# Kernel tuning notes

Measured on AMD Instinct MI355X. Metric: run time of the kernel, lower is better.

Reference implementation:

```python
import jax, jax.numpy as jnp
import numpy as np

N_HEAD = 4
D_K = 64
D_V = 64
D_MODEL = 256
LN_EPS = 1e-5


def setup_inputs() -> dict:
    key = jax.random.key(0)
    k1, k2, k3 = jax.random.split(key, 3)
    B, C, H, W = 2, D_MODEL, 64, 64
    q = jax.random.normal(k1, (B, C, H, W), dtype=jnp.float32)
    # w_qkvs: Linear(d_model, n_head*d_k, bias=False), weight [out, in]
    std_qkv = np.sqrt(2.0 / (D_MODEL + D_K))
    w_qkv = jax.random.normal(k2, (N_HEAD * D_K, D_MODEL), dtype=jnp.float32) * std_qkv
    # fc: Linear(n_head*d_v, d_model), xavier-normal-ish init
    std_fc = np.sqrt(2.0 / (N_HEAD * D_V + D_MODEL))
    fc_w = jax.random.normal(k3, (D_MODEL, N_HEAD * D_V), dtype=jnp.float32) * std_fc
    fc_b = jnp.zeros((D_MODEL,), dtype=jnp.float32)
    ln_g = jnp.ones((D_MODEL,), dtype=jnp.float32)
    ln_b = jnp.zeros((D_MODEL,), dtype=jnp.float32)
    return {"q": q, "w_qkv": w_qkv, "fc_w": fc_w, "fc_b": fc_b, "ln_g": ln_g, "ln_b": ln_b}


def reference(q, w_qkv, fc_w, fc_b, ln_g, ln_b):
    B, C, H, W = q.shape
    L = H * W
    # [B, C, H, W] -> [B, L, C]
    x = q.reshape(B, C, L).transpose(0, 2, 1)
    residual = x
    # shared QKV projection (self-attention branch: q == k == v)
    qkv = x @ w_qkv.T                                  # [B, L, nh*dk]
    qh = qkv.reshape(B, L, N_HEAD, D_K).transpose(2, 0, 1, 3)  # [h, B, L, dk]
    scale = jnp.asarray(np.sqrt(D_K), dtype=q.dtype)
    attn = jnp.einsum('hbqd,hbkd->hbqk', qh, qh) / scale       # [h, B, L, L]
    attn = jax.nn.softmax(attn, axis=-1)
    out = jnp.einsum('hbqk,hbkd->hbqd', attn, qh)              # [h, B, L, dv]
    # [h, B, L, dv] -> [B, L, h*dv]
    out = out.transpose(1, 2, 0, 3).reshape(B, L, N_HEAD * D_V)
    out = out @ fc_w.T + fc_b
    out = out + residual
    mu = jnp.mean(out, axis=-1, keepdims=True)
    var = jnp.mean(jnp.square(out - mu), axis=-1, keepdims=True)
    out = (out - mu) / jnp.sqrt(var + LN_EPS) * ln_g + ln_b
    # raw row-major view back to [B, C, H, W] (matches torch .view)
    return out.reshape(B, -1, H, W)
```

## Files before the change

### kernel.cpp

```cpp
#include <hip/hip_runtime.h>

#define L_SEQ 4096
#define DMODEL 256
#define DH 64
#define NKB 16

typedef __attribute__((ext_vector_type(8))) __bf16 bf16x8;
typedef __attribute__((ext_vector_type(4))) float f32x4;
typedef __attribute__((ext_vector_type(8))) unsigned short ushort8v;
typedef __attribute__((ext_vector_type(4))) unsigned short ushort4v;

__device__ __forceinline__ unsigned short f2bf(float f) {
  unsigned u = __builtin_bit_cast(unsigned, f);
  u += 0x7fffu + ((u >> 16) & 1u);
  return (unsigned short)(u >> 16);
}
__device__ __forceinline__ float bf2f(unsigned short h) {
  unsigned u = ((unsigned)h) << 16;
  return __builtin_bit_cast(float, u);
}
__device__ __forceinline__ bf16x8 ld_frag(const unsigned short* p) {
  return __builtin_bit_cast(bf16x8, *(const ushort8v*)p);
}

__global__ __launch_bounds__(256) void k_transpose(const float* __restrict__ q,
                                                   unsigned short* __restrict__ xbf,
                                                   const float* __restrict__ w,
                                                   const float* __restrict__ fcw,
                                                   unsigned short* __restrict__ wbf,
                                                   unsigned short* __restrict__ fcwbf) {
  int bx = blockIdx.x;
  int t = threadIdx.x;
  if (bx >= 512) {
    int i = ((bx - 512) * 256 + t) * 4;
    float4 a = *(const float4*)(w + i);
    float4 b = *(const float4*)(fcw + i);
    ushort4v av = {f2bf(a.x), f2bf(a.y), f2bf(a.z), f2bf(a.w)};
    ushort4v bv = {f2bf(b.x), f2bf(b.y), f2bf(b.z), f2bf(b.w)};
    *(ushort4v*)(wbf + i) = av;
    *(ushort4v*)(fcwbf + i) = bv;
    return;
  }
  __shared__ float T[64 * 65];
  int b = bx >> 8, rest = bx & 255;
  int ct = rest >> 6, lt = rest & 63;
#pragma unroll
  for (int it = 0; it < 4; ++it) {
    int i = (t >> 4) + it * 16;
    int j0 = (t & 15) * 4;
    float4 v = *(const float4*)(q + ((size_t)(b * 256 + ct * 64 + i)) * 4096 + lt * 64 + j0);
    T[i * 65 + j0 + 0] = v.x;
    T[i * 65 + j0 + 1] = v.y;
    T[i * 65 + j0 + 2] = v.z;
    T[i * 65 + j0 + 3] = v.w;
  }
  __syncthreads();
#pragma unroll
  for (int it = 0; it < 2; ++it) {
    int l = (t >> 3) + it * 32;
    int c0 = (t & 7) * 8;
    ushort8v o;
#pragma unroll
    for (int k = 0; k < 8; ++k) o[k] = f2bf(T[(c0 + k) * 65 + l]);
    *(ushort8v*)(xbf + ((size_t)(b * 4096 + lt * 64 + l)) * 256 + ct * 64 + c0) = o;
  }
}

#define KP2 136
__global__ __launch_bounds__(256) void k_qkv(const unsigned short* __restrict__ xbf,
                                             const unsigned short* __restrict__ wbf,
                                             unsigned short* __restrict__ Qh,
                                             unsigned short* __restrict__ QhT) {
  __shared__ unsigned short As[64 * KP2];
  __shared__ unsigned short Bs[64 * KP2];
  int bx = blockIdx.x;
  int mtile = bx >> 2, h = bx & 3;
  int m0 = mtile * 64;
  int b = m0 >> 12, l0 = m0 & 4095;
  int t = threadIdx.x;
  int wv = t >> 6, lane = t & 63, g = lane >> 4, ln = lane & 15;
  f32x4 acc[4] = {};
  for (int kb = 0; kb < 2; ++kb) {
#pragma unroll
    for (int it = 0; it < 4; ++it) {
      int idx = t + it * 256;
      int row = idx >> 4;
      int c0 = (idx & 15) * 8;
      *(ushort8v*)(As + row * KP2 + c0) =
          *(const ushort8v*)(xbf + (size_t)(m0 + row) * 256 + kb * 128 + c0);
      *(ushort8v*)(Bs + row * KP2 + c0) =
          *(const ushort8v*)(wbf + (size_t)(h * 64 + row) * 256 + kb * 128 + c0);
    }
    __syncthreads();
#pragma unroll
    for (int kc = 0; kc < 4; ++kc) {
      bf16x8 a = ld_frag(As + (wv * 16 + ln) * KP2 + kc * 32 + g * 8);
#pragma unroll
      for (int tn = 0; tn < 4; ++tn) {
        bf16x8 bb = ld_frag(Bs + (tn * 16 + ln) * KP2 + kc * 32 + g * 8);
        acc[tn] = __builtin_amdgcn_mfma_f32_16x16x32_bf16(a, bb, acc[tn], 0, 0, 0);
      }
    }
    __syncthreads();
  }
  size_t pbase = (size_t)(b * 4 + h);
#pragma unroll
  for (int tn = 0; tn < 4; ++tn) {
#pragma unroll
    for (int r = 0; r < 4; ++r) {
      int lrow = wv * 16 + g * 4 + r;
      int d = tn * 16 + ln;
      unsigned short bv = f2bf(acc[tn][r]);
      As[lrow * 64 + (((d >> 3) ^ (lrow & 7)) * 8) + (d & 7)] = bv;
      Bs[d * 64 + (((lrow >> 3) ^ (d & 7)) * 8) + (lrow & 7)] = bv;
    }
  }
#pragma unroll
  for (int s = 0; s < 2; ++s) {
    int flat = s * 64 + lane;
    int lrow = wv * 16 + (flat >> 3);
    int c8 = lane & 7;
    ushort8v v = *(const ushort8v*)(As + lrow * 64 + ((c8 ^ (lrow & 7)) * 8));
    *(ushort8v*)(Qh + (pbase * L_SEQ + l0 + lrow) * DH + c8 * 8) = v;
  }
  __syncthreads();
#pragma unroll
  for (int s = 0; s < 2; ++s) {
    int flat = s * 256 + t;
    int drow = flat >> 3;
    int c8 = t & 7;
    ushort8v v = *(const ushort8v*)(Bs + drow * 64 + ((c8 ^ (drow & 7)) * 8));
    *(ushort8v*)(QhT + (pbase * DH + drow) * L_SEQ + l0 + c8 * 8) = v;
  }
}

__global__ __launch_bounds__(256, 2) void k_attn(const unsigned short* __restrict__ Qh,
                                                 const unsigned short* __restrict__ QhT,
                                                 unsigned short* __restrict__ Opart,
                                                 float* __restrict__ Lpart) {
  __shared__ unsigned short Kt[64 * 64];
  __shared__ unsigned short Vt[64 * 64];
  __shared__ unsigned short Pb[256 * 64];
  int bx = blockIdx.x;
  int p = bx & 7;
  int u = bx >> 3;
  int qsup = u & 15, ks = u >> 4;
  int t = threadIdx.x;
  int wv = t >> 6, lane = t & 63, g = lane >> 4, ln = lane & 15;
  const unsigned short* Qp = Qh + (size_t)p * L_SEQ * DH;
  const unsigned short* QTp = QhT + (size_t)p * DH * L_SEQ;
  int q0 = qsup * 256;
  int qw = q0 + wv * 64;

  bf16x8 aQ[4][2];
#pragma unroll
  for (int nt = 0; nt < 4; ++nt)
#pragma unroll
    for (int kc = 0; kc < 2; ++kc)
      aQ[nt][kc] = ld_frag(Qp + (size_t)(qw + nt * 16 + ln) * DH + kc * 32 + g * 8);

  f32x4 oacc[4][4] = {};
  float lacc[4] = {0.f, 0.f, 0.f, 0.f};

  int srow0 = t >> 3, scol0 = t & 7;
  int srow1 = (t + 256) >> 3, scol1 = (t + 256) & 7;
  int sdst0 = srow0 * 64 + ((scol0 ^ (srow0 & 7)) * 8);
  int sdst1 = srow1 * 64 + ((scol1 ^ (srow1 & 7)) * 8);

  ushort8v kreg0, kreg1, vreg0, vreg1;
  {
    int kbase = (ks * NKB) * 64;
    kreg0 = *(const ushort8v*)(Qp + (size_t)(kbase + srow0) * DH + scol0 * 8);
    kreg1 = *(const ushort8v*)(Qp + (size_t)(kbase + srow1) * DH + scol1 * 8);
    vreg0 = *(const ushort8v*)(QTp + (size_t)srow0 * L_SEQ + kbase + scol0 * 8);
    vreg1 = *(const ushort8v*)(QTp + (size_t)srow1 * L_SEQ + kbase + scol1 * 8);
  }

  for (int kb = 0; kb < NKB; ++kb) {
    __syncthreads();
    *(ushort8v*)(Kt + sdst0) = kreg0;
    *(ushort8v*)(Kt + sdst1) = kreg1;
    *(ushort8v*)(Vt + sdst0) = vreg0;
    *(ushort8v*)(Vt + sdst1) = vreg1;
    __syncthreads();
    if (kb + 1 < NKB) {
      int kbase = (ks * NKB + kb + 1) * 64;
      kreg0 = *(const ushort8v*)(Qp + (size_t)(kbase + srow0) * DH + scol0 * 8);
      kreg1 = *(const ushort8v*)(Qp + (size_t)(kbase + srow1) * DH + scol1 * 8);
      vreg0 = *(const ushort8v*)(QTp + (size_t)srow0 * L_SEQ + kbase + scol0 * 8);
      vreg1 = *(const ushort8v*)(QTp + (size_t)srow1 * L_SEQ + kbase + scol1 * 8);
    }
#pragma unroll
    for (int mt = 0; mt < 4; ++mt) {
      int krow = mt * 16 + ln;
      bf16x8 aK0 = ld_frag(Kt + krow * 64 + (((0 * 4 + g) ^ (ln & 7)) * 8));
      bf16x8 aK1 = ld_frag(Kt + krow * 64 + (((1 * 4 + g) ^ (ln & 7)) * 8));
      f32x4 s[4] = {};
#pragma unroll
      for (int nt = 0; nt < 4; ++nt) {
        s[nt] = __builtin_amdgcn_mfma_f32_16x16x32_bf16(aK0, aQ[nt][0], s[nt], 0, 0, 0);
        s[nt] = __builtin_amdgcn_mfma_f32_16x16x32_bf16(aK1, aQ[nt][1], s[nt], 0, 0, 0);
      }
#pragma unroll
      for (int nt = 0; nt < 4; ++nt) {
        float p0 = __expf(fmaf(s[nt][0], 0.125f, -16.0f));
        float p1 = __expf(fmaf(s[nt][1], 0.125f, -16.0f));
        float p2 = __expf(fmaf(s[nt][2], 0.125f, -16.0f));
        float p3 = __expf(fmaf(s[nt][3], 0.125f, -16.0f));
        lacc[nt] += (p0 + p1) + (p2 + p3);
        ushort4v pk = {f2bf(p0), f2bf(p1), f2bf(p2), f2bf(p3)};
        int row = wv * 64 + nt * 16 + ln;
        int addr = row * 64 + (((2 * mt + (g >> 1)) ^ (ln & 7)) * 8) + (g & 1) * 4;
        *(ushort4v*)(Pb + addr) = pk;
      }
    }
#pragma unroll
    for (int kc = 0; kc < 2; ++kc) {
      bf16x8 bV[4];
#pragma unroll
      for (int tn = 0; tn < 4; ++tn)
        bV[tn] = ld_frag(Vt + (tn * 16 + ln) * 64 + (((kc * 4 + g) ^ (ln & 7)) * 8));
#pragma unroll
      for (int mq = 0; mq < 4; ++mq) {
        bf16x8 aP = ld_frag(Pb + (wv * 64 + mq * 16 + ln) * 64 + (((kc * 4 + g) ^ (ln & 7)) * 8));
#pragma unroll
        for (int tn = 0; tn < 4; ++tn)
          oacc[mq][tn] = __builtin_amdgcn_mfma_f32_16x16x32_bf16(aP, bV[tn], oacc[mq][tn], 0, 0, 0);
      }
    }
  }
#pragma unroll
  for (int nt = 0; nt < 4; ++nt) {
    lacc[nt] += __shfl_xor(lacc[nt], 16, 64);
    lacc[nt] += __shfl_xor(lacc[nt], 32, 64);
  }
  size_t pq = (size_t)(ks * 8 + p) * L_SEQ;
  if (g == 0) {
#pragma unroll
    for (int nt = 0; nt < 4; ++nt)
      __builtin_nontemporal_store(lacc[nt], &Lpart[pq + qw + nt * 16 + ln]);
  }
#pragma unroll
  for (int mq = 0; mq < 4; ++mq) {
#pragma unroll
    for (int r = 0; r < 4; ++r) {
      int row = wv * 64 + mq * 16 + g * 4 + r;
#pragma unroll
      for (int tn = 0; tn < 4; ++tn) {
        int d = tn * 16 + ln;
        Pb[row * 64 + (((d >> 3) ^ (row & 7)) * 8) + (d & 7)] = f2bf(oacc[mq][tn][r]);
      }
    }
  }
#pragma unroll
  for (int s = 0; s < 8; ++s) {
    int flat = s * 64 + lane;
    int row = wv * 64 + (flat >> 3);
    int c8 = lane & 7;
    ushort8v v = *(const ushort8v*)(Pb + row * 64 + ((c8 ^ (row & 7)) * 8));
    __builtin_nontemporal_store(v, (ushort8v*)(Opart + (pq + q0 + row) * DH + c8 * 8));
  }
}

#define CP 72
__global__ __launch_bounds__(256) void k_fc(const unsigned short* __restrict__ Opart,
                                            const float* __restrict__ Lpart,
                                            const unsigned short* __restrict__ fcwbf,
                                            const float* __restrict__ qres,
                                            const float* __restrict__ fcb,
                                            const float* __restrict__ lng,
                                            const float* __restrict__ lnb,
                                            float* __restrict__ out) {
  __shared__ unsigned short As[32 * CP];
  __shared__ unsigned short Bs[256 * CP];
  __shared__ float redS[4][32], redQ[4][32], muA[32], rsA[32];
  int bx = blockIdx.x;
  int m0 = bx * 32;
  int b = m0 >> 12, lpart = m0 & 4095;
  int t = threadIdx.x;
  int wv = t >> 6, lane = t & 63, g = lane >> 4, ln = lane & 15;
  f32x4 acc[2][4] = {};
  for (int kb = 0; kb < 4; ++kb) {
    {
      int row = t >> 3, c0 = (t & 7) * 8;
      int q = lpart + row;
      int p = b * 4 + kb;
      float lsum = __builtin_nontemporal_load(&Lpart[(size_t)(0 * 8 + p) * L_SEQ + q]) +
                   __builtin_nontemporal_load(&Lpart[(size_t)(1 * 8 + p) * L_SEQ + q]) +
                   __builtin_nontemporal_load(&Lpart[(size_t)(2 * 8 + p) * L_SEQ + q]) +
                   __builtin_nontemporal_load(&Lpart[(size_t)(3 * 8 + p) * L_SEQ + q]);
      float inv = 1.0f / lsum;
      float a8[8] = {0.f, 0.f, 0.f, 0.f, 0.f, 0.f, 0.f, 0.f};
#pragma unroll
      for (int ksp = 0; ksp < 4; ++ksp) {
        ushort8v v = __builtin_nontemporal_load(
            (const ushort8v*)(Opart + ((size_t)(ksp * 8 + p) * L_SEQ + q) * DH + c0));
#pragma unroll
        for (int j = 0; j < 8; ++j) a8[j] += bf2f(v[j]);
      }
      ushort8v o;
#pragma unroll
      for (int j = 0; j < 8; ++j) o[j] = f2bf(a8[j] * inv);
      *(ushort8v*)(As + row * CP + c0) = o;
    }
#pragma unroll
    for (int it = 0; it < 8; ++it) {
      int idx = t + it * 256;
      int row = idx >> 3, c0 = (idx & 7) * 8;
      *(ushort8v*)(Bs + row * CP + c0) =
          *(const ushort8v*)(fcwbf + (size_t)row * 256 + kb * 64 + c0);
    }
    __syncthreads();
#pragma unroll
    for (int kc = 0; kc < 2; ++kc) {
      bf16x8 a[2], bb[4];
#pragma unroll
      for (int mt = 0; mt < 2; ++mt) a[mt] = ld_frag(As + (mt * 16 + ln) * CP + kc * 32 + g * 8);
#pragma unroll
      for (int tn = 0; tn < 4; ++tn) bb[tn] = ld_frag(Bs + (wv * 64 + tn * 16 + ln) * CP + kc * 32 + g * 8);
#pragma unroll
      for (int mt = 0; mt < 2; ++mt)
#pragma unroll
        for (int tn = 0; tn < 4; ++tn)
          acc[mt][tn] = __builtin_amdgcn_mfma_f32_16x16x32_bf16(a[mt], bb[tn], acc[mt][tn], 0, 0, 0);
    }
    __syncthreads();
  }
  float fb[4], lg[4], lb[4];
#pragma unroll
  for (int tn = 0; tn < 4; ++tn) {
    int o = wv * 64 + tn * 16 + ln;
    fb[tn] = fcb[o]; lg[tn] = lng[o]; lb[tn] = lnb[o];
  }
#pragma unroll
  for (int mt = 0; mt < 2; ++mt) {
    float ps[4] = {0.f, 0.f, 0.f, 0.f}, pq2[4] = {0.f, 0.f, 0.f, 0.f};
#pragma unroll
    for (int tn = 0; tn < 4; ++tn) {
      int o = wv * 64 + tn * 16 + ln;
      float4 res = *(const float4*)(qres + ((size_t)(b * 256 + o)) * 4096 + lpart + mt * 16 + g * 4);
      float rv[4] = {res.x, res.y, res.z, res.w};
#pragma unroll
      for (int r = 0; r < 4; ++r) {
        float v = acc[mt][tn][r] + fb[tn] + rv[r];
        acc[mt][tn][r] = v;
        ps[r] += v;
        pq2[r] += v * v;
      }
    }
#pragma unroll
    for (int r = 0; r < 4; ++r) {
      float s = ps[r], q2 = pq2[r];
#pragma unroll
      for (int off = 1; off < 16; off <<= 1) {
        s += __shfl_xor(s, off, 64);
        q2 += __shfl_xor(q2, off, 64);
      }
      if (ln == 0) {
        int row = mt * 16 + g * 4 + r;
        redS[wv][row] = s;
        redQ[wv][row] = q2;
      }
    }
  }
  __syncthreads();
  if (t < 32) {
    float s = redS[0][t] + redS[1][t] + redS[2][t] + redS[3][t];
    float q2 = redQ[0][t] + redQ[1][t] + redQ[2][t] + redQ[3][t];
    float mu = s * (1.f / 256.f);
    float var = q2 * (1.f / 256.f) - mu * mu;
    muA[t] = mu;
    rsA[t] = rsqrtf(var + 1e-5f);
  }
  __syncthreads();
#pragma unroll
  for (int mt = 0; mt < 2; ++mt) {
#pragma unroll
    for (int r = 0; r < 4; ++r) {
      int row = mt * 16 + g * 4 + r;
      float mu = muA[row], rs = rsA[row];
#pragma unroll
      for (int tn = 0; tn < 4; ++tn) {
        int o = wv * 64 + tn * 16 + ln;
        out[(size_t)(m0 + row) * 256 + o] = (acc[mt][tn][r] - mu) * rs * lg[tn] + lb[tn];
      }
    }
  }
}

extern "C" void kernel_launch(void* const* d_in, const int* in_sizes, int n_in,
                              void* d_out, int out_size, void* d_ws, size_t ws_size,
                              hipStream_t stream) {
  const float* q = (const float*)d_in[0];
  const float* w_qkv = (const float*)d_in[1];
  const float* fc_w = (const float*)d_in[2];
  const float* fc_b = (const float*)d_in[3];
  const float* ln_g = (const float*)d_in[4];
  const float* ln_b = (const float*)d_in[5];
  float* out = (float*)d_out;

  unsigned short* wbf = (unsigned short*)d_ws;
  unsigned short* fcwbf = wbf + 65536;
  unsigned short* xbf = fcwbf + 65536;
  unsigned short* Qh = xbf + 2097152;
  unsigned short* QhT = Qh + 2097152;
  unsigned short* Opart = QhT + 2097152;
  float* Lpart = (float*)(Opart + 8388608);

  k_transpose<<<dim3(576), dim3(256), 0, stream>>>(q, xbf, w_qkv, fc_w, wbf, fcwbf);
  k_qkv<<<dim3(512), dim3(256), 0, stream>>>(xbf, wbf, Qh, QhT);
  k_attn<<<dim3(512), dim3(256), 0, stream>>>(Qh, QhT, Opart, Lpart);
  k_fc<<<dim3(256), dim3(256), 0, stream>>>(Opart, Lpart, fcwbf, q, fc_b, ln_g, ln_b, out);
}
```

Before: 139.3 us.

## Fuse transpose into QKV load, convert weights inline, add 8-way key split

Removes the separate transpose/convert kernel. The QKV GEMM now reads fp32 input directly, transposing and converting it to bf16 while staging into shared memory, and both GEMMs convert the fp32 weights on the fly. The attention key dimension is split across a KSPLIT template parameter. When workspace allows it uses 8 splits and 1024 blocks, which adds parallelism at the cost of more partial output traffic for the FC reduction. Software bf16 rounding is replaced with hardware vector conversions, and the transposing stores into shared memory use scalar 2-byte writes, which may cause bank conflicts.

```diff
diff --git a/kernel.cpp b/kernel.cpp
--- a/kernel.cpp
+++ b/kernel.cpp
@@ -3,72 +3,38 @@
 #define L_SEQ 4096
 #define DMODEL 256
 #define DH 64
-#define NKB 16
 
 typedef __attribute__((ext_vector_type(8))) __bf16 bf16x8;
+typedef __attribute__((ext_vector_type(4))) __bf16 bf16v4;
+typedef __attribute__((ext_vector_type(8))) __bf16 bf16v8;
 typedef __attribute__((ext_vector_type(4))) float f32x4;
+typedef __attribute__((ext_vector_type(8))) float f32x8;
 typedef __attribute__((ext_vector_type(8))) unsigned short ushort8v;
 typedef __attribute__((ext_vector_type(4))) unsigned short ushort4v;
 
-__device__ __forceinline__ unsigned short f2bf(float f) {
-  unsigned u = __builtin_bit_cast(unsigned, f);
-  u += 0x7fffu + ((u >> 16) & 1u);
-  return (unsigned short)(u >> 16);
-}
 __device__ __forceinline__ float bf2f(unsigned short h) {
   unsigned u = ((unsigned)h) << 16;
   return __builtin_bit_cast(float, u);
 }
+__device__ __forceinline__ ushort4v cvt4(float a, float b, float c, float d) {
+  bf16v4 h = __builtin_convertvector((f32x4){a, b, c, d}, bf16v4);
+  return __builtin_bit_cast(ushort4v, h);
+}
+__device__ __forceinline__ ushort8v cvt8(f32x8 v) {
+  bf16v8 h = __builtin_convertvector(v, bf16v8);
+  return __builtin_bit_cast(ushort8v, h);
+}
+__device__ __forceinline__ unsigned short f2bf(float f) {
+  __bf16 h = (__bf16)f;
+  return __builtin_bit_cast(unsigned short, h);
+}
 __device__ __forceinline__ bf16x8 ld_frag(const unsigned short* p) {
   return __builtin_bit_cast(bf16x8, *(const ushort8v*)p);
 }
 
-__global__ __launch_bounds__(256) void k_transpose(const float* __restrict__ q,
-                                                   unsigned short* __restrict__ xbf,
-                                                   const float* __restrict__ w,
-                                                   const float* __restrict__ fcw,
-                                                   unsigned short* __restrict__ wbf,
-                                                   unsigned short* __restrict__ fcwbf) {
-  int bx = blockIdx.x;
-  int t = threadIdx.x;
-  if (bx >= 512) {
-    int i = ((bx - 512) * 256 + t) * 4;
-    float4 a = *(const float4*)(w + i);
-    float4 b = *(const float4*)(fcw + i);
-    ushort4v av = {f2bf(a.x), f2bf(a.y), f2bf(a.z), f2bf(a.w)};
-    ushort4v bv = {f2bf(b.x), f2bf(b.y), f2bf(b.z), f2bf(b.w)};
-    *(ushort4v*)(wbf + i) = av;
-    *(ushort4v*)(fcwbf + i) = bv;
-    return;
-  }
-  __shared__ float T[64 * 65];
-  int b = bx >> 8, rest = bx & 255;
-  int ct = rest >> 6, lt = rest & 63;
-#pragma unroll
-  for (int it = 0; it < 4; ++it) {
-    int i = (t >> 4) + it * 16;
-    int j0 = (t & 15) * 4;
-    float4 v = *(const float4*)(q + ((size_t)(b * 256 + ct * 64 + i)) * 4096 + lt * 64 + j0);
-    T[i * 65 + j0 + 0] = v.x;
-    T[i * 65 + j0 + 1] = v.y;
-    T[i * 65 + j0 + 2] = v.z;
-    T[i * 65 + j0 + 3] = v.w;
-  }
-  __syncthreads();
-#pragma unroll
-  for (int it = 0; it < 2; ++it) {
-    int l = (t >> 3) + it * 32;
-    int c0 = (t & 7) * 8;
-    ushort8v o;
-#pragma unroll
-    for (int k = 0; k < 8; ++k) o[k] = f2bf(T[(c0 + k) * 65 + l]);
-    *(ushort8v*)(xbf + ((size_t)(b * 4096 + lt * 64 + l)) * 256 + ct * 64 + c0) = o;
-  }
-}
-
 #define KP2 136
-__global__ __launch_bounds__(256) void k_qkv(const unsigned short* __restrict__ xbf,
-                                             const unsigned short* __restrict__ wbf,
+__global__ __launch_bounds__(256) void k_qkv(const float* __restrict__ q,
+                                             const float* __restrict__ w,
                                              unsigned short* __restrict__ Qh,
                                              unsigned short* __restrict__ QhT) {
   __shared__ unsigned short As[64 * KP2];
@@ -82,14 +48,26 @@
   f32x4 acc[4] = {};
   for (int kb = 0; kb < 2; ++kb) {
 #pragma unroll
+    for (int it = 0; it < 8; ++it) {
+      int idx = t + it * 256;
+      int cl = idx & 127;
+      int lq = idx >> 7;
+      float4 v = *(const float4*)(q + ((size_t)(b * 256 + kb * 128 + cl)) * 4096 + l0 + lq * 4);
+      As[(lq * 4 + 0) * KP2 + cl] = f2bf(v.x);
+      As[(lq * 4 + 1) * KP2 + cl] = f2bf(v.y);
+      As[(lq * 4 + 2) * KP2 + cl] = f2bf(v.z);
+      As[(lq * 4 + 3) * KP2 + cl] = f2bf(v.w);
+    }
+#pragma unroll
     for (int it = 0; it < 4; ++it) {
       int idx = t + it * 256;
       int row = idx >> 4;
-      int c0 = (idx & 15) * 8;
-      *(ushort8v*)(As + row * KP2 + c0) =
-          *(const ushort8v*)(xbf + (size_t)(m0 + row) * 256 + kb * 128 + c0);
-      *(ushort8v*)(Bs + row * KP2 + c0) =
-          *(const ushort8v*)(wbf + (size_t)(h * 64 + row) * 256 + kb * 128 + c0);
+      int c8 = (idx & 15) * 8;
+      const float* src = w + (size_t)(h * 64 + row) * 256 + kb * 128 + c8;
+      float4 v0 = *(const float4*)(src);
+      float4 v1 = *(const float4*)(src + 4);
+      *(ushort8v*)(Bs + row * KP2 + c8) =
+          cvt8((f32x8){v0.x, v0.y, v0.z, v0.w, v1.x, v1.y, v1.z, v1.w});
     }
     __syncthreads();
 #pragma unroll
@@ -134,10 +112,12 @@
   }
 }
 
+template <int KSPLIT>
 __global__ __launch_bounds__(256, 2) void k_attn(const unsigned short* __restrict__ Qh,
                                                  const unsigned short* __restrict__ QhT,
                                                  unsigned short* __restrict__ Opart,
                                                  float* __restrict__ Lpart) {
+  const int NKB = 64 / KSPLIT;
   __shared__ unsigned short Kt[64 * 64];
   __shared__ unsigned short Vt[64 * 64];
   __shared__ unsigned short Pb[256 * 64];
@@ -208,7 +188,7 @@
         float p2 = __expf(fmaf(s[nt][2], 0.125f, -16.0f));
         float p3 = __expf(fmaf(s[nt][3], 0.125f, -16.0f));
         lacc[nt] += (p0 + p1) + (p2 + p3);
-        ushort4v pk = {f2bf(p0), f2bf(p1), f2bf(p2), f2bf(p3)};
+        ushort4v pk = cvt4(p0, p1, p2, p3);
         int row = wv * 64 + nt * 16 + ln;
         int addr = row * 64 + (((2 * mt + (g >> 1)) ^ (ln & 7)) * 8) + (g & 1) * 4;
         *(ushort4v*)(Pb + addr) = pk;
@@ -263,9 +243,10 @@
 }
 
 #define CP 72
+template <int KSPLIT>
 __global__ __launch_bounds__(256) void k_fc(const unsigned short* __restrict__ Opart,
                                             const float* __restrict__ Lpart,
-                                            const unsigned short* __restrict__ fcwbf,
+                                            const float* __restrict__ fcw,
                                             const float* __restrict__ qres,
                                             const float* __restrict__ fcb,
                                             const float* __restrict__ lng,
@@ -283,32 +264,34 @@
   for (int kb = 0; kb < 4; ++kb) {
     {
       int row = t >> 3, c0 = (t & 7) * 8;
-      int q = lpart + row;
+      int qrow = lpart + row;
       int p = b * 4 + kb;
-      float lsum = __builtin_nontemporal_load(&Lpart[(size_t)(0 * 8 + p) * L_SEQ + q]) +
-                   __builtin_nontemporal_load(&Lpart[(size_t)(1 * 8 + p) * L_SEQ + q]) +
-                   __builtin_nontemporal_load(&Lpart[(size_t)(2 * 8 + p) * L_SEQ + q]) +
-                   __builtin_nontemporal_load(&Lpart[(size_t)(3 * 8 + p) * L_SEQ + q]);
+      float lsum = 0.f;
+#pragma unroll
+      for (int ksp = 0; ksp < KSPLIT; ++ksp)
+        lsum += __builtin_nontemporal_load(&Lpart[(size_t)(ksp * 8 + p) * L_SEQ + qrow]);
       float inv = 1.0f / lsum;
       float a8[8] = {0.f, 0.f, 0.f, 0.f, 0.f, 0.f, 0.f, 0.f};
 #pragma unroll
-      for (int ksp = 0; ksp < 4; ++ksp) {
+      for (int ksp = 0; ksp < KSPLIT; ++ksp) {
         ushort8v v = __builtin_nontemporal_load(
-            (const ushort8v*)(Opart + ((size_t)(ksp * 8 + p) * L_SEQ + q) * DH + c0));
+            (const ushort8v*)(Opart + ((size_t)(ksp * 8 + p) * L_SEQ + qrow) * DH + c0));
 #pragma unroll
         for (int j = 0; j < 8; ++j) a8[j] += bf2f(v[j]);
       }
-      ushort8v o;
-#pragma unroll
-      for (int j = 0; j < 8; ++j) o[j] = f2bf(a8[j] * inv);
-      *(ushort8v*)(As + row * CP + c0) = o;
+      *(ushort8v*)(As + row * CP + c0) =
+          cvt8((f32x8){a8[0] * inv, a8[1] * inv, a8[2] * inv, a8[3] * inv,
+                       a8[4] * inv, a8[5] * inv, a8[6] * inv, a8[7] * inv});
     }
 #pragma unroll
     for (int it = 0; it < 8; ++it) {
       int idx = t + it * 256;
       int row = idx >> 3, c0 = (idx & 7) * 8;
+      const float* src = fcw + (size_t)row * 256 + kb * 64 + c0;
+      float4 v0 = *(const float4*)(src);
+      float4 v1 = *(const float4*)(src + 4);
       *(ushort8v*)(Bs + row * CP + c0) =
-          *(const ushort8v*)(fcwbf + (size_t)row * 256 + kb * 64 + c0);
+          cvt8((f32x8){v0.x, v0.y, v0.z, v0.w, v1.x, v1.y, v1.z, v1.w});
     }
     __syncthreads();
 #pragma unroll
@@ -399,16 +382,20 @@
   const float* ln_b = (const float*)d_in[5];
   float* out = (float*)d_out;
 
-  unsigned short* wbf = (unsigned short*)d_ws;
-  unsigned short* fcwbf = wbf + 65536;
-  unsigned short* xbf = fcwbf + 65536;
-  unsigned short* Qh = xbf + 2097152;
+  unsigned short* Qh = (unsigned short*)d_ws;
   unsigned short* QhT = Qh + 2097152;
   unsigned short* Opart = QhT + 2097152;
-  float* Lpart = (float*)(Opart + 8388608);
-
-  k_transpose<<<dim3(576), dim3(256), 0, stream>>>(q, xbf, w_qkv, fc_w, wbf, fcwbf);
-  k_qkv<<<dim3(512), dim3(256), 0, stream>>>(xbf, wbf, Qh, QhT);
-  k_attn<<<dim3(512), dim3(256), 0, stream>>>(Qh, QhT, Opart, Lpart);
-  k_fc<<<dim3(256), dim3(256), 0, stream>>>(Opart, Lpart, fcwbf, q, fc_b, ln_g, ln_b, out);
-}
+
+  size_t need8 = (size_t)2 * 2097152 * 2 + (size_t)8 * 8 * 4096 * 64 * 2 + (size_t)8 * 8 * 4096 * 4;
+
+  k_qkv<<<dim3(512), dim3(256), 0, stream>>>(q, w_qkv, Qh, QhT);
+  if (ws_size >= need8) {
+    float* Lpart = (float*)(Opart + (size_t)8 * 8 * 4096 * 64);
+    k_attn<8><<<dim3(1024), dim3(256), 0, stream>>>(Qh, QhT, Opart, Lpart);
+    k_fc<8><<<dim3(256), dim3(256), 0, stream>>>(Opart, Lpart, fc_w, q, fc_b, ln_g, ln_b, out);
+  } else {
+    float* Lpart = (float*)(Opart + (size_t)4 * 8 * 4096 * 64);
+    k_attn<4><<<dim3(512), dim3(256), 0, stream>>>(Qh, QhT, Opart, Lpart);
+    k_fc<4><<<dim3(256), dim3(256), 0, stream>>>(Opart, Lpart, fc_w, q, fc_b, ln_g, ln_b, out);
+  }
+}
```

After: 156.1 us. 1.12x slower.
